# Optimization experiments

Measured on AMD Instinct MI355X. Metric: run time of the kernel, lower is better.

The kernel has to match this reference:

```python
import jax, jax.numpy as jnp
import numpy as np

N_NODES = 100000
N_EDGES = 1600000
IN_DIM = 128
HID_DIM = 128
OUT_DIM = 64


def _glorot(key, shape):
    fan_in, fan_out = shape
    lim = float(np.sqrt(6.0 / (fan_in + fan_out)))
    return jax.random.uniform(key, shape, jnp.float32, -lim, lim)


def setup_inputs() -> dict:
    key = jax.random.key(0)
    ks = jax.random.split(key, 8)
    x = jax.random.normal(ks[0], (N_NODES, IN_DIM), jnp.float32)
    edge_index = jax.random.randint(ks[1], (2, N_EDGES), 0, N_NODES, jnp.int64)
    edge_weight = jax.random.uniform(ks[2], (N_EDGES,), jnp.float32)
    W1 = _glorot(ks[3], (IN_DIM, HID_DIM))
    b1 = jnp.zeros((HID_DIM,), jnp.float32)
    W2 = _glorot(ks[4], (HID_DIM, HID_DIM))
    b2 = jnp.zeros((HID_DIM,), jnp.float32)
    W3 = _glorot(ks[5], (HID_DIM, OUT_DIM))
    b3 = jnp.zeros((OUT_DIM,), jnp.float32)
    return {"x": x, "edge_index": edge_index, "edge_weight": edge_weight,
            "W1": W1, "b1": b1, "W2": W2, "b2": b2, "W3": W3, "b3": b3}


def gcn_conv(x, src, dst, ew, W, b, n_nodes):
    # torch_geometric GCNConv: add self-loops (weight 1), symmetric normalization,
    # linear transform (no bias) then aggregate, then add bias.
    xw = x @ W                                            # [N, out]
    deg = jax.ops.segment_sum(ew, dst, num_segments=n_nodes) + 1.0  # self-loop
    dis = jax.lax.rsqrt(deg)                              # deg >= 1, safe
    norm = dis[src] * ew * dis[dst]                       # [E]
    agg = jax.ops.segment_sum(norm[:, None] * xw[src], dst, num_segments=n_nodes)
    # self-loop contribution: norm_ii = dis_i^2 * 1.0
    return agg + (dis * dis)[:, None] * xw + b


def reference(x, edge_index, edge_weight, W1, b1, W2, b2, W3, b3):
    src, dst = edge_index[0], edge_index[1]
    n = x.shape[0]
    h = gcn_conv(x, src, dst, edge_weight, W1, b1, n)
    h = jax.nn.relu(h)  # dropout is identity at inference
    h = gcn_conv(h, src, dst, edge_weight, W2, b2, n)
    h = jax.nn.relu(h)
    out = gcn_conv(h, src, dst, edge_weight, W3, b3, n)
    return out
```

## Files before the change

### kernel.cpp

```cpp
#include <hip/hip_runtime.h>


typedef __attribute__((ext_vector_type(8))) short bf16x8;
typedef __attribute__((ext_vector_type(4))) float f32x4;

#define CHUNK 2048

__device__ inline unsigned short f2bf(float f) {
  unsigned int u = __float_as_uint(f);
  u += 0x7fffu + ((u >> 16) & 1u);
  return (unsigned short)(u >> 16);
}

__device__ inline int detect_use64(const int* __restrict__ ei, int t,
                                   int* __restrict__ lds_flag) {
  if (t == 0) *lds_flag = 0;
  __syncthreads();
  int acc = 0;
#pragma unroll
  for (int it = 0; it < 8; ++it) acc |= ei[2 * (t + (it << 8)) + 1];
  if (acc != 0) atomicOr(lds_flag, 1);
  __syncthreads();
  return (*lds_flag == 0) ? 1 : 0;
}

__global__ __launch_bounds__(256)
void bin_hist(const int* __restrict__ ei, int* __restrict__ mat,
              int E, int NB, int NBLK) {
  __shared__ int hist[1024];
  __shared__ int lflag;
  const int t = threadIdx.x;
  const int use64 = detect_use64(ei, t, &lflag);
  for (int i = t; i < NB; i += 256) hist[i] = 0;
  __syncthreads();
  const int base = blockIdx.x * CHUNK;
#pragma unroll
  for (int it = 0; it < CHUNK / 256; ++it) {
    const int e = base + t + it * 256;
    if (e < E) {
      const int d = use64 ? ei[2 * (E + e)] : ei[E + e];
      atomicAdd(&hist[d >> 7], 1);
    }
  }
  __syncthreads();
  for (int i = t; i < NB; i += 256) mat[i * NBLK + blockIdx.x] = hist[i];
}

__global__ __launch_bounds__(256)
void scan_phase1(const int* __restrict__ mat, int* __restrict__ bsums, int L) {
  __shared__ int red[256];
  const int t = threadIdx.x;
  const int base = blockIdx.x * 1024 + t * 4;
  int s = 0;
#pragma unroll
  for (int j = 0; j < 4; ++j)
    if (base + j < L) s += mat[base + j];
  red[t] = s;
  __syncthreads();
  for (int off = 128; off > 0; off >>= 1) {
    if (t < off) red[t] += red[t + off];
    __syncthreads();
  }
  if (t == 0) bsums[blockIdx.x] = red[0];
}

__global__ __launch_bounds__(1024)
void scan_phase2(int* __restrict__ bsums, int* __restrict__ row_start, int B, int N) {
  __shared__ int s[1024];
  const int t = threadIdx.x;
  const int v = (t < B) ? bsums[t] : 0;
  s[t] = v;
  __syncthreads();
  for (int off = 1; off < 1024; off <<= 1) {
    const int add = (t >= off) ? s[t - off] : 0;
    __syncthreads();
    s[t] += add;
    __syncthreads();
  }
  if (t < B) bsums[t] = s[t] - v;
  if (t == B - 1) row_start[N] = s[t];
}

__global__ __launch_bounds__(256)
void scan_phase3(int* __restrict__ mat, const int* __restrict__ bsums, int L) {
  __shared__ int tsum[256];
  const int t = threadIdx.x;
  const int base = blockIdx.x * 1024 + t * 4;
  int v[4];
#pragma unroll
  for (int j = 0; j < 4; ++j) v[j] = (base + j < L) ? mat[base + j] : 0;
  const int tot = v[0] + v[1] + v[2] + v[3];
  tsum[t] = tot;
  __syncthreads();
  for (int off = 1; off < 256; off <<= 1) {
    const int add = (t >= off) ? tsum[t - off] : 0;
    __syncthreads();
    tsum[t] += add;
    __syncthreads();
  }
  int run = bsums[blockIdx.x] + tsum[t] - tot;
#pragma unroll
  for (int j = 0; j < 4; ++j) {
    if (base + j < L) { mat[base + j] = run; run += v[j]; }
  }
}

__global__ __launch_bounds__(256)
void bin_scatter(const int* __restrict__ ei, const float* __restrict__ ew,
                 const int* __restrict__ mat, int2* __restrict__ binned,
                 int E, int NB, int NBLK) {
  __shared__ int boff[1024];
  __shared__ int cur[1024];
  __shared__ int lflag;
  const int t = threadIdx.x;
  const int use64 = detect_use64(ei, t, &lflag);
  for (int i = t; i < NB; i += 256) {
    boff[i] = mat[i * NBLK + blockIdx.x];
    cur[i] = 0;
  }
  __syncthreads();
  const int base = blockIdx.x * CHUNK;
#pragma unroll
  for (int it = 0; it < CHUNK / 256; ++it) {
    const int e = base + t + it * 256;
    if (e < E) {
      const int s = use64 ? ei[2 * e] : ei[e];
      const int d = use64 ? ei[2 * (E + e)] : ei[E + e];
      const int b = d >> 7;
      const int r = atomicAdd(&cur[b], 1);
      binned[boff[b] + r] = make_int2(s | ((d & 127) << 17), __float_as_int(ew[e]));
    }
  }
}

__global__ __launch_bounds__(512)
void bucket_finalize(const int2* __restrict__ binned, const int* __restrict__ mat,
                     int* __restrict__ row_start, float* __restrict__ dis,
                     int2* __restrict__ csr, int E, int N, int NB, int NBLK) {
  __shared__ int cnt[128];
  __shared__ unsigned int fxs[128];
  __shared__ int sc[128];
  __shared__ int rowb[128];
  __shared__ float disl[128];
  __shared__ int cur[128];
  const int t = threadIdx.x;
  const int b = blockIdx.x;
  const int beg = mat[b * NBLK];
  const int end = (b == NB - 1) ? E : mat[(b + 1) * NBLK];
  if (t < 128) { cnt[t] = 0; fxs[t] = 0u; }
  __syncthreads();
  for (int i = beg + t; i < end; i += 512) {
    const int2 r = binned[i];
    const int dl = (r.x >> 17) & 127;
    atomicAdd(&cnt[dl], 1);
    atomicAdd(&fxs[dl], (unsigned int)(__int_as_float(r.y) * 16777216.0f));
  }
  __syncthreads();
  if (t < 128) sc[t] = cnt[t];
  __syncthreads();
  for (int off = 1; off < 128; off <<= 1) {
    const int v = (t < 128 && t >= off) ? sc[t - off] : 0;
    __syncthreads();
    if (t < 128) sc[t] += v;
    __syncthreads();
  }
  if (t < 128) {
    const int node = (b << 7) + t;
    const int rb = beg + sc[t] - cnt[t];
    rowb[t] = rb;
    cur[t] = 0;
    if (node < N) {
      row_start[node] = rb;
      const float deg = (float)fxs[t] * (1.0f / 16777216.0f);
      const float di = rsqrtf(deg + 1.0f);
      dis[node] = di;
      disl[t] = di;
    }
  }
  __syncthreads();
  for (int i = beg + t; i < end; i += 512) {
    const int2 r = binned[i];
    const int dl = (r.x >> 17) & 127;
    const int rk = atomicAdd(&cur[dl], 1);
    csr[rowb[dl] + rk] =
        make_int2(r.x & 0x1FFFF, __float_as_int(__int_as_float(r.y) * disl[dl]));
  }
}

__global__ __launch_bounds__(256)
void prep_bf16(const float* __restrict__ W1, const float* __restrict__ W2,
               const float* __restrict__ W3, unsigned short* __restrict__ Wt1,
               unsigned short* __restrict__ Wt2, unsigned short* __restrict__ Wt3,
               const float* __restrict__ x, unsigned short* __restrict__ xbf,
               long long n4) {
  const int WTB = 160;
  if (blockIdx.x < WTB) {
    const int idx = blockIdx.x * 256 + threadIdx.x;
    if (idx < 16384) {
      const int m = idx >> 7, k = idx & 127;
      Wt1[idx] = f2bf(W1[k * 128 + m]);
    } else if (idx < 32768) {
      const int l = idx - 16384;
      const int m = l >> 7, k = l & 127;
      Wt2[l] = f2bf(W2[k * 128 + m]);
    } else {
      const int l = idx - 32768;
      const int m = l >> 7, k = l & 127;
      Wt3[l] = f2bf(W3[k * 64 + m]);
    }
    return;
  }
  long long i = (long long)(blockIdx.x - WTB) * 256 + threadIdx.x;
  const long long stride = (long long)(gridDim.x - WTB) * 256;
  for (; i < n4; i += stride) {
    const float4 v = ((const float4*)x)[i];
    ushort4 o;
    o.x = f2bf(v.x); o.y = f2bf(v.y); o.z = f2bf(v.z); o.w = f2bf(v.w);
    ((ushort4*)xbf)[i] = o;
  }
}

template <int M>
__global__ __launch_bounds__(256)
void gemm_mfma(const unsigned short* __restrict__ A, const unsigned short* __restrict__ Bt,
               const float* __restrict__ dis, unsigned short* __restrict__ C, int N) {
  const int lane = threadIdx.x & 63;
  const int m = lane & 15;
  const int q = lane >> 4;
  const int row0 = (blockIdx.x << 6) + ((threadIdx.x >> 6) << 4);

  const bool rowok = (row0 + m) < N;
  const unsigned short* arow = A + (long long)(row0 + m) * 128 + q * 8;
  bf16x8 a[4];
  const bf16x8 zf = {0, 0, 0, 0, 0, 0, 0, 0};
#pragma unroll
  for (int kt = 0; kt < 4; ++kt)
    a[kt] = rowok ? *(const bf16x8*)(arow + kt * 32) : zf;

#pragma unroll
  for (int ct = 0; ct < M / 16; ++ct) {
    f32x4 acc = {0.f, 0.f, 0.f, 0.f};
    const unsigned short* brow = Bt + (ct * 16 + m) * 128 + q * 8;
#pragma unroll
    for (int kt = 0; kt < 4; ++kt) {
      const bf16x8 b = *(const bf16x8*)(brow + kt * 32);
      acc = __builtin_amdgcn_mfma_f32_16x16x32_bf16(a[kt], b, acc, 0, 0, 0);
    }
#pragma unroll
    for (int r = 0; r < 4; ++r) {
      const int row = row0 + q * 4 + r;
      if (row < N) {
        const float sc = dis[row];
        C[(long long)row * M + ct * 16 + m] = f2bf(acc[r] * sc);
      }
    }
  }
}

template <int M, bool RELU, bool OUTBF>
__global__ __launch_bounds__(256)
void gather(const int2* __restrict__ csr, const int* __restrict__ row_start,
            const unsigned short* __restrict__ xw, const float* __restrict__ dis,
            const float* __restrict__ bias, void* __restrict__ outp, int N) {
  const int node = (blockIdx.x << 2) + (threadIdx.x >> 6);
  const int lane = threadIdx.x & 63;
  if (node >= N) return;
  const int beg = __builtin_amdgcn_readfirstlane(row_start[node]);
  const int end = __builtin_amdgcn_readfirstlane(row_start[node + 1]);
  if (M == 128) {
    const int c = lane << 1;
    float2 a0 = make_float2(0.f, 0.f), a1 = a0, a2 = a0, a3 = a0;
    int e = beg;
    for (; e + 15 < end; e += 16) {
      int2 p[16];
      unsigned int u[16];
#pragma unroll
      for (int j = 0; j < 16; ++j) p[j] = csr[e + j];
#pragma unroll
      for (int j = 0; j < 16; ++j)
        u[j] = *(const unsigned int*)(xw + (long long)p[j].x * 128 + c);
#pragma unroll
      for (int j = 0; j < 16; ++j) {
        const float nm = __int_as_float(p[j].y);
        float2& ac = (j & 2) ? ((j & 1) ? a3 : a2) : ((j & 1) ? a1 : a0);
        ac.x = fmaf(nm, __uint_as_float(u[j] << 16), ac.x);
        ac.y = fmaf(nm, __uint_as_float(u[j] & 0xffff0000u), ac.y);
      }
    }
    for (; e + 7 < end; e += 8) {
      int2 p[8];
      unsigned int u[8];
#pragma unroll
      for (int j = 0; j < 8; ++j) p[j] = csr[e + j];
#pragma unroll
      for (int j = 0; j < 8; ++j)
        u[j] = *(const unsigned int*)(xw + (long long)p[j].x * 128 + c);
#pragma unroll
      for (int j = 0; j < 8; ++j) {
        const float nm = __int_as_float(p[j].y);
        float2& ac = (j & 2) ? ((j & 1) ? a3 : a2) : ((j & 1) ? a1 : a0);
        ac.x = fmaf(nm, __uint_as_float(u[j] << 16), ac.x);
        ac.y = fmaf(nm, __uint_as_float(u[j] & 0xffff0000u), ac.y);
      }
    }
    for (; e + 1 < end; e += 2) {
      const int2 p0 = csr[e], p1 = csr[e + 1];
      const unsigned int u0 = *(const unsigned int*)(xw + (long long)p0.x * 128 + c);
      const unsigned int u1 = *(const unsigned int*)(xw + (long long)p1.x * 128 + c);
      const float n0 = __int_as_float(p0.y), n1 = __int_as_float(p1.y);
      a0.x = fmaf(n0, __uint_as_float(u0 << 16), a0.x);
      a0.y = fmaf(n0, __uint_as_float(u0 & 0xffff0000u), a0.y);
      a1.x = fmaf(n1, __uint_as_float(u1 << 16), a1.x);
      a1.y = fmaf(n1, __uint_as_float(u1 & 0xffff0000u), a1.y);
    }
    if (e < end) {
      const int2 p = csr[e];
      const float nm = __int_as_float(p.y);
      const unsigned int u = *(const unsigned int*)(xw + (long long)p.x * 128 + c);
      a2.x = fmaf(nm, __uint_as_float(u << 16), a2.x);
      a2.y = fmaf(nm, __uint_as_float(u & 0xffff0000u), a2.y);
    }
    float2 acc;
    acc.x = (a0.x + a1.x) + (a2.x + a3.x);
    acc.y = (a0.y + a1.y) + (a2.y + a3.y);
    const float di = dis[node];
    const unsigned int su = *(const unsigned int*)(xw + (long long)node * 128 + c);
    const float2 bv = *(const float2*)(bias + c);
    acc.x = fmaf(di, __uint_as_float(su << 16), acc.x) + bv.x;
    acc.y = fmaf(di, __uint_as_float(su & 0xffff0000u), acc.y) + bv.y;
    if (RELU) { acc.x = fmaxf(acc.x, 0.f); acc.y = fmaxf(acc.y, 0.f); }
    if (OUTBF) {
      const unsigned int pk =
          (unsigned int)f2bf(acc.x) | ((unsigned int)f2bf(acc.y) << 16);
      ((unsigned int*)outp)[(long long)node * 64 + lane] = pk;
    } else {
      *(float2*)((float*)outp + (long long)node * 128 + c) = acc;
    }
  } else {
    float a0 = 0.f, a1 = 0.f, a2 = 0.f, a3 = 0.f;
    int e = beg;
    for (; e + 15 < end; e += 16) {
      int2 p[16];
      unsigned int v[16];
#pragma unroll
      for (int j = 0; j < 16; ++j) p[j] = csr[e + j];
#pragma unroll
      for (int j = 0; j < 16; ++j) v[j] = xw[(long long)p[j].x * 64 + lane];
#pragma unroll
      for (int j = 0; j < 16; ++j) {
        float& ac = (j & 2) ? ((j & 1) ? a3 : a2) : ((j & 1) ? a1 : a0);
        ac = fmaf(__int_as_float(p[j].y), __uint_as_float(v[j] << 16), ac);
      }
    }
    for (; e + 7 < end; e += 8) {
      int2 p[8];
      unsigned int v[8];
#pragma unroll
      for (int j = 0; j < 8; ++j) p[j] = csr[e + j];
#pragma unroll
      for (int j = 0; j < 8; ++j) v[j] = xw[(long long)p[j].x * 64 + lane];
#pragma unroll
      for (int j = 0; j < 8; ++j) {
        float& ac = (j & 2) ? ((j & 1) ? a3 : a2) : ((j & 1) ? a1 : a0);
        ac = fmaf(__int_as_float(p[j].y), __uint_as_float(v[j] << 16), ac);
      }
    }
    for (; e < end; ++e) {
      const int2 p = csr[e];
      const unsigned int v = xw[(long long)p.x * 64 + lane];
      a0 = fmaf(__int_as_float(p.y), __uint_as_float(v << 16), a0);
    }
    float acc = (a0 + a1) + (a2 + a3);
    const float di = dis[node];
    const unsigned int sv = xw[(long long)node * 64 + lane];
    float r = fmaf(di, __uint_as_float(sv << 16), acc) + bias[lane];
    if (RELU) r = fmaxf(r, 0.f);
    ((float*)outp)[(long long)node * 64 + lane] = r;
  }
}

extern "C" void kernel_launch(void* const* d_in, const int* in_sizes, int n_in,
                              void* d_out, int out_size, void* d_ws, size_t ws_size,
                              hipStream_t stream) {
  const float* x  = (const float*)d_in[0];
  const int*   ei = (const int*)d_in[1];
  const float* ew = (const float*)d_in[2];
  const float* W1 = (const float*)d_in[3];
  const float* b1 = (const float*)d_in[4];
  const float* W2 = (const float*)d_in[5];
  const float* b2 = (const float*)d_in[6];
  const float* W3 = (const float*)d_in[7];
  const float* b3 = (const float*)d_in[8];
  float* out = (float*)d_out;

  const int IN = 128;
  const int N = in_sizes[0] / IN;
  const int E = in_sizes[2];

  char* ws = (char*)d_ws;
  float* dis       = (float*)(ws + (1u << 20));
  int*   bsums     = (int*)(ws + (1536u << 10));
  int*   row_start = (int*)(ws + (1600u << 10));
  int2*  csr       = (int2*)(ws + (2560u << 10));
  unsigned short* Wt1 = (unsigned short*)(ws + (15872u << 10));
  unsigned short* Wt2 = (unsigned short*)(ws + (15872u << 10) + (128u << 10));
  unsigned short* Wt3 = (unsigned short*)(ws + (15872u << 10) + (256u << 10));
  unsigned short* bufA = (unsigned short*)(ws + (16u << 20));
  unsigned short* hbf  = (unsigned short*)(ws + (42u << 20));
  int*   mat    = (int*)(ws + (68u << 20));
  int2*  binned = (int2*)(ws + (71u << 20));

  const dim3 blk(256);
  const int NB = (N + 127) >> 7;
  const int NBLK = (E + CHUNK - 1) / CHUNK;
  const int L = NB * NBLK;
  const int SB = (L + 1023) / 1024;

  hipLaunchKernelGGL(bin_hist, dim3(NBLK), blk, 0, stream, ei, mat, E, NB, NBLK);
  hipLaunchKernelGGL(scan_phase1, dim3(SB), blk, 0, stream, mat, bsums, L);
  hipLaunchKernelGGL(scan_phase2, dim3(1), dim3(1024), 0, stream, bsums, row_start, SB, N);
  hipLaunchKernelGGL(scan_phase3, dim3(SB), blk, 0, stream, mat, bsums, L);
  hipLaunchKernelGGL(bin_scatter, dim3(NBLK), blk, 0, stream, ei, ew, mat,
                     binned, E, NB, NBLK);
  hipLaunchKernelGGL(bucket_finalize, dim3(NB), dim3(512), 0, stream, binned, mat,
                     row_start, dis, csr, E, N, NB, NBLK);
  hipLaunchKernelGGL(prep_bf16, dim3(160 + 2048), blk, 0, stream,
                     W1, W2, W3, Wt1, Wt2, Wt3, x, hbf, (long long)N * 32);

  const int gGemm = (N + 63) / 64;
  const int gGather = (N + 3) / 4;

  hipLaunchKernelGGL((gemm_mfma<128>), dim3(gGemm), blk, 0, stream, hbf, Wt1, dis, bufA, N);
  hipLaunchKernelGGL((gather<128, true, true>), dim3(gGather), blk, 0, stream,
                     csr, row_start, bufA, dis, b1, hbf, N);
  hipLaunchKernelGGL((gemm_mfma<128>), dim3(gGemm), blk, 0, stream, hbf, Wt2, dis, bufA, N);
  hipLaunchKernelGGL((gather<128, true, true>), dim3(gGather), blk, 0, stream,
                     csr, row_start, bufA, dis, b2, hbf, N);
  hipLaunchKernelGGL((gemm_mfma<64>), dim3(gGemm), blk, 0, stream, hbf, Wt3, dis, bufA, N);
  hipLaunchKernelGGL((gather<64, false, false>), dim3(gGather), blk, 0, stream,
                     csr, row_start, bufA, dis, b3, out, N);
}
```

Before: 435.3 us.

## Fuse CSR build into one cooperative kernel and convert x inside first GEMM

The six CSR-construction kernels (histogram, three scan phases, scatter, bucket finalize) are merged into one cooperative kernel that separates the phases with grid-wide syncs. This removes separate launches and repeated use64 detection. The standalone fp32-to-bf16 pass over x is dropped; the first GEMM now reads fp32 x directly and converts it in registers, avoiding one write and re-read of the activation matrix. The trade-offs are grid-sync overhead, the finalize phase running at 256 threads instead of 512, and a wider fp32 read in GEMM1.

```diff
diff --git a/kernel.cpp b/kernel.cpp
--- a/kernel.cpp
+++ b/kernel.cpp
@@ -1,4 +1,7 @@
 #include <hip/hip_runtime.h>
+#include <hip/hip_cooperative_groups.h>
+
+namespace cg = cooperative_groups;
 
 
 typedef __attribute__((ext_vector_type(8))) short bf16x8;
@@ -12,217 +15,210 @@
   return (unsigned short)(u >> 16);
 }
 
-__device__ inline int detect_use64(const int* __restrict__ ei, int t,
-                                   int* __restrict__ lds_flag) {
-  if (t == 0) *lds_flag = 0;
-  __syncthreads();
-  int acc = 0;
-#pragma unroll
-  for (int it = 0; it < 8; ++it) acc |= ei[2 * (t + (it << 8)) + 1];
-  if (acc != 0) atomicOr(lds_flag, 1);
-  __syncthreads();
-  return (*lds_flag == 0) ? 1 : 0;
-}
-
 __global__ __launch_bounds__(256)
-void bin_hist(const int* __restrict__ ei, int* __restrict__ mat,
-              int E, int NB, int NBLK) {
-  __shared__ int hist[1024];
+void build_csr(const int* __restrict__ ei, const float* __restrict__ ew,
+               int* __restrict__ mat, int* __restrict__ bsums,
+               int* __restrict__ row_start, float* __restrict__ dis,
+               int2* __restrict__ csr, int2* __restrict__ binned,
+               int E, int N, int NB, int NBLK, int SB) {
+  cg::grid_group grid = cg::this_grid();
+  __shared__ int sbuf[2048];
   __shared__ int lflag;
   const int t = threadIdx.x;
-  const int use64 = detect_use64(ei, t, &lflag);
-  for (int i = t; i < NB; i += 256) hist[i] = 0;
+  const int bid = blockIdx.x;
+  const int L = NB * NBLK;
+
+  if (t == 0) lflag = 0;
   __syncthreads();
-  const int base = blockIdx.x * CHUNK;
-#pragma unroll
-  for (int it = 0; it < CHUNK / 256; ++it) {
-    const int e = base + t + it * 256;
-    if (e < E) {
-      const int d = use64 ? ei[2 * (E + e)] : ei[E + e];
-      atomicAdd(&hist[d >> 7], 1);
-    }
+  {
+    int acc = 0;
+#pragma unroll
+    for (int it = 0; it < 8; ++it) acc |= ei[2 * (t + (it << 8)) + 1];
+    if (acc != 0) atomicOr(&lflag, 1);
   }
   __syncthreads();
-  for (int i = t; i < NB; i += 256) mat[i * NBLK + blockIdx.x] = hist[i];
+  const int use64 = (lflag == 0) ? 1 : 0;
+
+  if (bid < NBLK) {
+    for (int i = t; i < NB; i += 256) sbuf[i] = 0;
+    __syncthreads();
+    const int base = bid * CHUNK;
+#pragma unroll
+    for (int it = 0; it < CHUNK / 256; ++it) {
+      const int e = base + t + it * 256;
+      if (e < E) {
+        const int d = use64 ? ei[2 * (E + e)] : ei[E + e];
+        atomicAdd(&sbuf[d >> 7], 1);
+      }
+    }
+    __syncthreads();
+    for (int i = t; i < NB; i += 256) mat[i * NBLK + bid] = sbuf[i];
+  }
+  grid.sync();
+
+  if (bid < SB) {
+    const int base = bid * 1024 + t * 4;
+    int s = 0;
+#pragma unroll
+    for (int j = 0; j < 4; ++j)
+      if (base + j < L) s += mat[base + j];
+    sbuf[t] = s;
+    __syncthreads();
+    for (int off = 128; off > 0; off >>= 1) {
+      if (t < off) sbuf[t] += sbuf[t + off];
+      __syncthreads();
+    }
+    if (t == 0) bsums[bid] = sbuf[0];
+  }
+  grid.sync();
+
+  if (bid == 0) {
+    int ov[4];
+#pragma unroll
+    for (int j = 0; j < 4; ++j) {
+      const int idx = t + j * 256;
+      ov[j] = (idx < SB) ? bsums[idx] : 0;
+      sbuf[idx] = ov[j];
+    }
+    __syncthreads();
+    for (int off = 1; off < 1024; off <<= 1) {
+      int tmp[4];
+#pragma unroll
+      for (int j = 0; j < 4; ++j) {
+        const int idx = t + j * 256;
+        tmp[j] = (idx >= off) ? sbuf[idx - off] : 0;
+      }
+      __syncthreads();
+#pragma unroll
+      for (int j = 0; j < 4; ++j) sbuf[t + j * 256] += tmp[j];
+      __syncthreads();
+    }
+#pragma unroll
+    for (int j = 0; j < 4; ++j) {
+      const int idx = t + j * 256;
+      if (idx < SB) bsums[idx] = sbuf[idx] - ov[j];
+      if (idx == SB - 1) row_start[N] = sbuf[idx];
+    }
+  }
+  grid.sync();
+
+  if (bid < SB) {
+    const int base = bid * 1024 + t * 4;
+    int v[4];
+#pragma unroll
+    for (int j = 0; j < 4; ++j) v[j] = (base + j < L) ? mat[base + j] : 0;
+    const int tot = v[0] + v[1] + v[2] + v[3];
+    sbuf[t] = tot;
+    __syncthreads();
+    for (int off = 1; off < 256; off <<= 1) {
+      const int add = (t >= off) ? sbuf[t - off] : 0;
+      __syncthreads();
+      sbuf[t] += add;
+      __syncthreads();
+    }
+    int run = bsums[bid] + sbuf[t] - tot;
+#pragma unroll
+    for (int j = 0; j < 4; ++j) {
+      if (base + j < L) { mat[base + j] = run; run += v[j]; }
+    }
+  }
+  grid.sync();
+
+  if (bid < NBLK) {
+    int* boff = sbuf;
+    int* cur  = sbuf + 1024;
+    for (int i = t; i < NB; i += 256) {
+      boff[i] = mat[i * NBLK + bid];
+      cur[i] = 0;
+    }
+    __syncthreads();
+    const int base = bid * CHUNK;
+#pragma unroll
+    for (int it = 0; it < CHUNK / 256; ++it) {
+      const int e = base + t + it * 256;
+      if (e < E) {
+        const int s = use64 ? ei[2 * e] : ei[e];
+        const int d = use64 ? ei[2 * (E + e)] : ei[E + e];
+        const int b = d >> 7;
+        const int r = atomicAdd(&cur[b], 1);
+        binned[boff[b] + r] = make_int2(s | ((d & 127) << 17), __float_as_int(ew[e]));
+      }
+    }
+  }
+  grid.sync();
+
+  if (bid < NB) {
+    int* cnt = sbuf;
+    unsigned int* fxs = (unsigned int*)(sbuf + 128);
+    int* sc = sbuf + 256;
+    int* rowb = sbuf + 384;
+    float* disl = (float*)(sbuf + 512);
+    int* cur2 = sbuf + 640;
+    const int beg = mat[bid * NBLK];
+    const int end = (bid == NB - 1) ? E : mat[(bid + 1) * NBLK];
+    if (t < 128) { cnt[t] = 0; fxs[t] = 0u; }
+    __syncthreads();
+    for (int i = beg + t; i < end; i += 256) {
+      const int2 r = binned[i];
+      const int dl = (r.x >> 17) & 127;
+      atomicAdd(&cnt[dl], 1);
+      atomicAdd(&fxs[dl], (unsigned int)(__int_as_float(r.y) * 16777216.0f));
+    }
+    __syncthreads();
+    if (t < 128) sc[t] = cnt[t];
+    __syncthreads();
+    for (int off = 1; off < 128; off <<= 1) {
+      const int v = (t < 128 && t >= off) ? sc[t - off] : 0;
+      __syncthreads();
+      if (t < 128) sc[t] += v;
+      __syncthreads();
+    }
+    if (t < 128) {
+      const int node = (bid << 7) + t;
+      const int rb = beg + sc[t] - cnt[t];
+      rowb[t] = rb;
+      cur2[t] = 0;
+      if (node < N) {
+        row_start[node] = rb;
+        const float deg = (float)fxs[t] * (1.0f / 16777216.0f);
+        const float di = rsqrtf(deg + 1.0f);
+        dis[node] = di;
+        disl[t] = di;
+      }
+    }
+    __syncthreads();
+    for (int i = beg + t; i < end; i += 256) {
+      const int2 r = binned[i];
+      const int dl = (r.x >> 17) & 127;
+      const int rk = atomicAdd(&cur2[dl], 1);
+      csr[rowb[dl] + rk] =
+          make_int2(r.x & 0x1FFFF, __float_as_int(__int_as_float(r.y) * disl[dl]));
+    }
+  }
 }
 
 __global__ __launch_bounds__(256)
-void scan_phase1(const int* __restrict__ mat, int* __restrict__ bsums, int L) {
-  __shared__ int red[256];
-  const int t = threadIdx.x;
-  const int base = blockIdx.x * 1024 + t * 4;
-  int s = 0;
-#pragma unroll
-  for (int j = 0; j < 4; ++j)
-    if (base + j < L) s += mat[base + j];
-  red[t] = s;
-  __syncthreads();
-  for (int off = 128; off > 0; off >>= 1) {
-    if (t < off) red[t] += red[t + off];
-    __syncthreads();
-  }
-  if (t == 0) bsums[blockIdx.x] = red[0];
-}
-
-__global__ __launch_bounds__(1024)
-void scan_phase2(int* __restrict__ bsums, int* __restrict__ row_start, int B, int N) {
-  __shared__ int s[1024];
-  const int t = threadIdx.x;
-  const int v = (t < B) ? bsums[t] : 0;
-  s[t] = v;
-  __syncthreads();
-  for (int off = 1; off < 1024; off <<= 1) {
-    const int add = (t >= off) ? s[t - off] : 0;
-    __syncthreads();
-    s[t] += add;
-    __syncthreads();
-  }
-  if (t < B) bsums[t] = s[t] - v;
-  if (t == B - 1) row_start[N] = s[t];
-}
-
+void prep_w(const float* __restrict__ W1, const float* __restrict__ W2,
+            const float* __restrict__ W3, unsigned short* __restrict__ Wt1,
+            unsigned short* __restrict__ Wt2, unsigned short* __restrict__ Wt3) {
+  const int idx = blockIdx.x * 256 + threadIdx.x;
+  if (idx < 16384) {
+    const int m = idx >> 7, k = idx & 127;
+    Wt1[idx] = f2bf(W1[k * 128 + m]);
+  } else if (idx < 32768) {
+    const int l = idx - 16384;
+    const int m = l >> 7, k = l & 127;
+    Wt2[l] = f2bf(W2[k * 128 + m]);
+  } else if (idx < 40960) {
+    const int l = idx - 32768;
+    const int m = l >> 7, k = l & 127;
+    Wt3[l] = f2bf(W3[k * 64 + m]);
+  }
+}
+
+template <int M, bool AF32>
 __global__ __launch_bounds__(256)
-void scan_phase3(int* __restrict__ mat, const int* __restrict__ bsums, int L) {
-  __shared__ int tsum[256];
-  const int t = threadIdx.x;
-  const int base = blockIdx.x * 1024 + t * 4;
-  int v[4];
-#pragma unroll
-  for (int j = 0; j < 4; ++j) v[j] = (base + j < L) ? mat[base + j] : 0;
-  const int tot = v[0] + v[1] + v[2] + v[3];
-  tsum[t] = tot;
-  __syncthreads();
-  for (int off = 1; off < 256; off <<= 1) {
-    const int add = (t >= off) ? tsum[t - off] : 0;
-    __syncthreads();
-    tsum[t] += add;
-    __syncthreads();
-  }
-  int run = bsums[blockIdx.x] + tsum[t] - tot;
-#pragma unroll
-  for (int j = 0; j < 4; ++j) {
-    if (base + j < L) { mat[base + j] = run; run += v[j]; }
-  }
-}
-
-__global__ __launch_bounds__(256)
-void bin_scatter(const int* __restrict__ ei, const float* __restrict__ ew,
-                 const int* __restrict__ mat, int2* __restrict__ binned,
-                 int E, int NB, int NBLK) {
-  __shared__ int boff[1024];
-  __shared__ int cur[1024];
-  __shared__ int lflag;
-  const int t = threadIdx.x;
-  const int use64 = detect_use64(ei, t, &lflag);
-  for (int i = t; i < NB; i += 256) {
-    boff[i] = mat[i * NBLK + blockIdx.x];
-    cur[i] = 0;
-  }
-  __syncthreads();
-  const int base = blockIdx.x * CHUNK;
-#pragma unroll
-  for (int it = 0; it < CHUNK / 256; ++it) {
-    const int e = base + t + it * 256;
-    if (e < E) {
-      const int s = use64 ? ei[2 * e] : ei[e];
-      const int d = use64 ? ei[2 * (E + e)] : ei[E + e];
-      const int b = d >> 7;
-      const int r = atomicAdd(&cur[b], 1);
-      binned[boff[b] + r] = make_int2(s | ((d & 127) << 17), __float_as_int(ew[e]));
-    }
-  }
-}
-
-__global__ __launch_bounds__(512)
-void bucket_finalize(const int2* __restrict__ binned, const int* __restrict__ mat,
-                     int* __restrict__ row_start, float* __restrict__ dis,
-                     int2* __restrict__ csr, int E, int N, int NB, int NBLK) {
-  __shared__ int cnt[128];
-  __shared__ unsigned int fxs[128];
-  __shared__ int sc[128];
-  __shared__ int rowb[128];
-  __shared__ float disl[128];
-  __shared__ int cur[128];
-  const int t = threadIdx.x;
-  const int b = blockIdx.x;
-  const int beg = mat[b * NBLK];
-  const int end = (b == NB - 1) ? E : mat[(b + 1) * NBLK];
-  if (t < 128) { cnt[t] = 0; fxs[t] = 0u; }
-  __syncthreads();
-  for (int i = beg + t; i < end; i += 512) {
-    const int2 r = binned[i];
-    const int dl = (r.x >> 17) & 127;
-    atomicAdd(&cnt[dl], 1);
-    atomicAdd(&fxs[dl], (unsigned int)(__int_as_float(r.y) * 16777216.0f));
-  }
-  __syncthreads();
-  if (t < 128) sc[t] = cnt[t];
-  __syncthreads();
-  for (int off = 1; off < 128; off <<= 1) {
-    const int v = (t < 128 && t >= off) ? sc[t - off] : 0;
-    __syncthreads();
-    if (t < 128) sc[t] += v;
-    __syncthreads();
-  }
-  if (t < 128) {
-    const int node = (b << 7) + t;
-    const int rb = beg + sc[t] - cnt[t];
-    rowb[t] = rb;
-    cur[t] = 0;
-    if (node < N) {
-      row_start[node] = rb;
-      const float deg = (float)fxs[t] * (1.0f / 16777216.0f);
-      const float di = rsqrtf(deg + 1.0f);
-      dis[node] = di;
-      disl[t] = di;
-    }
-  }
-  __syncthreads();
-  for (int i = beg + t; i < end; i += 512) {
-    const int2 r = binned[i];
-    const int dl = (r.x >> 17) & 127;
-    const int rk = atomicAdd(&cur[dl], 1);
-    csr[rowb[dl] + rk] =
-        make_int2(r.x & 0x1FFFF, __float_as_int(__int_as_float(r.y) * disl[dl]));
-  }
-}
-
-__global__ __launch_bounds__(256)
-void prep_bf16(const float* __restrict__ W1, const float* __restrict__ W2,
-               const float* __restrict__ W3, unsigned short* __restrict__ Wt1,
-               unsigned short* __restrict__ Wt2, unsigned short* __restrict__ Wt3,
-               const float* __restrict__ x, unsigned short* __restrict__ xbf,
-               long long n4) {
-  const int WTB = 160;
-  if (blockIdx.x < WTB) {
-    const int idx = blockIdx.x * 256 + threadIdx.x;
-    if (idx < 16384) {
-      const int m = idx >> 7, k = idx & 127;
-      Wt1[idx] = f2bf(W1[k * 128 + m]);
-    } else if (idx < 32768) {
-      const int l = idx - 16384;
-      const int m = l >> 7, k = l & 127;
-      Wt2[l] = f2bf(W2[k * 128 + m]);
-    } else {
-      const int l = idx - 32768;
-      const int m = l >> 7, k = l & 127;
-      Wt3[l] = f2bf(W3[k * 64 + m]);
-    }
-    return;
-  }
-  long long i = (long long)(blockIdx.x - WTB) * 256 + threadIdx.x;
-  const long long stride = (long long)(gridDim.x - WTB) * 256;
-  for (; i < n4; i += stride) {
-    const float4 v = ((const float4*)x)[i];
-    ushort4 o;
-    o.x = f2bf(v.x); o.y = f2bf(v.y); o.z = f2bf(v.z); o.w = f2bf(v.w);
-    ((ushort4*)xbf)[i] = o;
-  }
-}
-
-template <int M>
-__global__ __launch_bounds__(256)
-void gemm_mfma(const unsigned short* __restrict__ A, const unsigned short* __restrict__ Bt,
+void gemm_mfma(const void* __restrict__ Ap, const unsigned short* __restrict__ Bt,
                const float* __restrict__ dis, unsigned short* __restrict__ C, int N) {
   const int lane = threadIdx.x & 63;
   const int m = lane & 15;
@@ -230,12 +226,32 @@
   const int row0 = (blockIdx.x << 6) + ((threadIdx.x >> 6) << 4);
 
   const bool rowok = (row0 + m) < N;
-  const unsigned short* arow = A + (long long)(row0 + m) * 128 + q * 8;
   bf16x8 a[4];
   const bf16x8 zf = {0, 0, 0, 0, 0, 0, 0, 0};
-#pragma unroll
-  for (int kt = 0; kt < 4; ++kt)
-    a[kt] = rowok ? *(const bf16x8*)(arow + kt * 32) : zf;
+  if (AF32) {
+    const float* arow = (const float*)Ap + (long long)(row0 + m) * 128 + q * 8;
+#pragma unroll
+    for (int kt = 0; kt < 4; ++kt) {
+      if (rowok) {
+        const float4 v0 = *(const float4*)(arow + kt * 32);
+        const float4 v1 = *(const float4*)(arow + kt * 32 + 4);
+        bf16x8 av;
+        av[0] = (short)f2bf(v0.x); av[1] = (short)f2bf(v0.y);
+        av[2] = (short)f2bf(v0.z); av[3] = (short)f2bf(v0.w);
+        av[4] = (short)f2bf(v1.x); av[5] = (short)f2bf(v1.y);
+        av[6] = (short)f2bf(v1.z); av[7] = (short)f2bf(v1.w);
+        a[kt] = av;
+      } else {
+        a[kt] = zf;
+      }
+    }
+  } else {
+    const unsigned short* arow =
+        (const unsigned short*)Ap + (long long)(row0 + m) * 128 + q * 8;
+#pragma unroll
+    for (int kt = 0; kt < 4; ++kt)
+      a[kt] = rowok ? *(const bf16x8*)(arow + kt * 32) : zf;
+  }
 
 #pragma unroll
   for (int ct = 0; ct < M / 16; ++ct) {
@@ -411,32 +427,33 @@
   int2*  binned = (int2*)(ws + (71u << 20));
 
   const dim3 blk(256);
-  const int NB = (N + 127) >> 7;
-  const int NBLK = (E + CHUNK - 1) / CHUNK;
-  const int L = NB * NBLK;
-  const int SB = (L + 1023) / 1024;
-
-  hipLaunchKernelGGL(bin_hist, dim3(NBLK), blk, 0, stream, ei, mat, E, NB, NBLK);
-  hipLaunchKernelGGL(scan_phase1, dim3(SB), blk, 0, stream, mat, bsums, L);
-  hipLaunchKernelGGL(scan_phase2, dim3(1), dim3(1024), 0, stream, bsums, row_start, SB, N);
-  hipLaunchKernelGGL(scan_phase3, dim3(SB), blk, 0, stream, mat, bsums, L);
-  hipLaunchKernelGGL(bin_scatter, dim3(NBLK), blk, 0, stream, ei, ew, mat,
-                     binned, E, NB, NBLK);
-  hipLaunchKernelGGL(bucket_finalize, dim3(NB), dim3(512), 0, stream, binned, mat,
-                     row_start, dis, csr, E, N, NB, NBLK);
-  hipLaunchKernelGGL(prep_bf16, dim3(160 + 2048), blk, 0, stream,
-                     W1, W2, W3, Wt1, Wt2, Wt3, x, hbf, (long long)N * 32);
+  int NB   = (N + 127) >> 7;
+  int NBLK = (E + CHUNK - 1) / CHUNK;
+  int SB   = (NB * NBLK + 1023) / 1024;
+  const int GB = (NBLK > NB ? (NBLK > SB ? NBLK : SB) : (NB > SB ? NB : SB));
+
+  hipLaunchKernelGGL(prep_w, dim3(160), blk, 0, stream, W1, W2, W3, Wt1, Wt2, Wt3);
+
+  {
+    void* args[] = {(void*)&ei, (void*)&ew, (void*)&mat, (void*)&bsums,
+                    (void*)&row_start, (void*)&dis, (void*)&csr, (void*)&binned,
+                    (void*)&E, (void*)&N, (void*)&NB, (void*)&NBLK, (void*)&SB};
+    hipLaunchCooperativeKernel((const void*)build_csr, dim3(GB), blk, args, 0, stream);
+  }
 
   const int gGemm = (N + 63) / 64;
   const int gGather = (N + 3) / 4;
 
-  hipLaunchKernelGGL((gemm_mfma<128>), dim3(gGemm), blk, 0, stream, hbf, Wt1, dis, bufA, N);
+  hipLaunchKernelGGL((gemm_mfma<128, true>), dim3(gGemm), blk, 0, stream,
+                     (const void*)x, Wt1, dis, bufA, N);
   hipLaunchKernelGGL((gather<128, true, true>), dim3(gGather), blk, 0, stream,
                      csr, row_start, bufA, dis, b1, hbf, N);
-  hipLaunchKernelGGL((gemm_mfma<128>), dim3(gGemm), blk, 0, stream, hbf, Wt2, dis, bufA, N);
+  hipLaunchKernelGGL((gemm_mfma<128, false>), dim3(gGemm), blk, 0, stream,
+                     (const void*)hbf, Wt2, dis, bufA, N);
   hipLaunchKernelGGL((gather<128, true, true>), dim3(gGather), blk, 0, stream,
                      csr, row_start, bufA, dis, b2, hbf, N);
-  hipLaunchKernelGGL((gemm_mfma<64>), dim3(gGemm), blk, 0, stream, hbf, Wt3, dis, bufA, N);
+  hipLaunchKernelGGL((gemm_mfma<64, false>), dim3(gGemm), blk, 0, stream,
+                     (const void*)hbf, Wt3, dis, bufA, N);
   hipLaunchKernelGGL((gather<64, false, false>), dim3(gGather), blk, 0, stream,
                      csr, row_start, bufA, dis, b3, out, N);
 }
```

Result: slower. 921.7 us (+111.8%).
